# Optimization experiments

Measured on AMD Instinct MI355X. Metric: run time of the kernel, lower is better.

## Reference

```python
import math
import jax, jax.numpy as jnp
import numpy as np

EPS = 1.0
B, T, D, H = 8, 512, 768, 12
DH = D // H  # 64


def setup_inputs() -> dict:
    key = jax.random.key(0)
    ks = jax.random.split(key, 10)
    std = 0.02
    return {
        "x": jax.random.normal(ks[0], (B, T, D), dtype=jnp.float32),
        "r_position_embedding": jax.random.normal(ks[1], (T, D), dtype=jnp.float32),
        "r_content_bias": jax.random.normal(ks[2], (H, DH), dtype=jnp.float32),
        "r_position_bias": jax.random.normal(ks[3], (H, DH), dtype=jnp.float32),
        # Conv1D(linear) params, stored as (in, out) so y = x @ W + b
        "Wqkv": jax.random.normal(ks[4], (D, 3 * D), dtype=jnp.float32) * std,
        "bqkv": jnp.zeros((3 * D,), dtype=jnp.float32),
        "Wh": jax.random.normal(ks[5], (D, D), dtype=jnp.float32) * std,
        "bh": jnp.zeros((D,), dtype=jnp.float32),
        "Wp": jax.random.normal(ks[6], (D, D), dtype=jnp.float32) * std,
        "bp": jnp.zeros((D,), dtype=jnp.float32),
    }


def reference(x, r_position_embedding, r_content_bias, r_position_bias,
              Wqkv, bqkv, Wh, bh, Wp, bp):
    # QKV projection and head split
    qkv = x @ Wqkv + bqkv                                   # (B,T,3D)
    q, k, v = jnp.split(qkv, 3, axis=-1)
    split_heads = lambda t: t.reshape(B, T, H, DH).transpose(0, 2, 1, 3)  # (B,H,T,DH)
    q, k, v = split_heads(q), split_heads(k), split_heads(v)

    # content scores
    scores = jnp.einsum('bhtd,bhsd->bhts', q, k)            # (B,H,T,T)

    # relative position projection: linear is row-wise, so project once then gather.
    # rel_pos[c, r] = linear_position(pos_emb[max(0, c - r)])
    proj = (r_position_embedding @ Wp + bp).reshape(T, H, DH)  # (P=T, H, DH)
    idx = jnp.maximum(0, jnp.arange(T)[:, None] - jnp.arange(T)[None, :])  # (T,T) = max(0, c-r)

    # q . rel_pos term: compute vs all P distinct positions, then gather per (c, r)
    rel_q = jnp.einsum('bhtd,phd->bhtp', q, proj)           # (B,H,T,P)
    scores = scores + jnp.take_along_axis(rel_q, idx[None, None, :, :], axis=-1)

    # content-bias and position-bias terms (query-independent)
    bias_c = jnp.einsum('hd,phd->hp', r_content_bias, proj)[:, idx]   # (H,T,T)
    bias_p = jnp.einsum('hd,phd->hp', r_position_bias, proj)[:, idx]  # (H,T,T)
    scores = scores + bias_c[None] + bias_p[None]

    # masked softmax with EPS=1 quirks (faithful to original)
    scores = scores / (math.sqrt(DH) + EPS)
    mask = jnp.tril(jnp.ones((T, T), dtype=jnp.float32))    # causal
    masked_exps = jnp.exp(scores) * mask
    att = masked_exps / (masked_exps.sum(-1, keepdims=True) + 2.0 * EPS)

    ctx = jnp.einsum('bhts,bhsd->bhtd', att, v)             # (B,H,T,DH)
    # original: permute(0,2,3,1) then flatten -> (B,T,DH*H) interleaving (d, h)
    ctx = ctx.transpose(0, 2, 3, 1).reshape(B, T, D)
    out = ctx @ Wh + bh
    k_out = k.transpose(0, 1, 3, 2)                         # (B,H,DH,T) as module returns
    return out, k_out, v
```

## Files before the change

### kernel.cpp

```cpp
#include <hip/hip_runtime.h>
#include <hip/hip_bf16.h>


#define NT 512
#define ND 768
#define NH 12

typedef short short4_t __attribute__((ext_vector_type(4)));
typedef short short8_t __attribute__((ext_vector_type(8)));
typedef float float4_t __attribute__((ext_vector_type(4)));

__device__ __forceinline__ float b2f(unsigned short u) {
    union { unsigned int i; float f; } x; x.i = ((unsigned int)u) << 16; return x.f;
}
__device__ __forceinline__ unsigned short f2b(float f) {
    union { float f; unsigned int i; } x; x.f = f;
    unsigned int i = x.i;
    i += 0x7fffu + ((i >> 16) & 1u);
    return (unsigned short)(i >> 16);
}

__global__ __launch_bounds__(256) void cvt_b(const float* __restrict__ in,
                                             unsigned short* __restrict__ out, int n8)
{
    const int i = blockIdx.x * 256 + threadIdx.x;
    if (i >= n8) return;
    const float* s = in + (size_t)i * 8;
    float4_t f0 = *(const float4_t*)s;
    float4_t f1 = *(const float4_t*)(s + 4);
    union { short8_t v; unsigned short u[8]; } pk;
    pk.u[0] = f2b(f0[0]); pk.u[1] = f2b(f0[1]); pk.u[2] = f2b(f0[2]); pk.u[3] = f2b(f0[3]);
    pk.u[4] = f2b(f1[0]); pk.u[5] = f2b(f1[1]); pk.u[6] = f2b(f1[2]); pk.u[7] = f2b(f1[3]);
    *(short8_t*)&out[(size_t)i * 8] = pk.v;
}

__global__ __launch_bounds__(256) void transp_b(const float* __restrict__ in,
                                                unsigned short* __restrict__ out,
                                                int K, int N)
{
    __shared__ float t[32][33];
    const int k0 = blockIdx.y * 32;
    const int n0 = blockIdx.x * 32;
    const int r  = threadIdx.x >> 3;
    const int c  = (threadIdx.x & 7) * 4;
    float4_t v = *(const float4_t*)&in[(size_t)(k0 + r) * N + n0 + c];
    t[r][c + 0] = v[0]; t[r][c + 1] = v[1]; t[r][c + 2] = v[2]; t[r][c + 3] = v[3];
    __syncthreads();
    union { short4_t v; unsigned short u[4]; } pk;
    pk.u[0] = f2b(t[c + 0][r]);
    pk.u[1] = f2b(t[c + 1][r]);
    pk.u[2] = f2b(t[c + 2][r]);
    pk.u[3] = f2b(t[c + 3][r]);
    *(short4_t*)&out[(size_t)(n0 + r) * K + k0 + c] = pk.v;
}

template <int MODE>
__global__ __launch_bounds__(256) void gemm128(
    const unsigned short* __restrict__ A, const unsigned short* __restrict__ BT,
    const float* __restrict__ biasf,
    unsigned short* __restrict__ ob0, float* __restrict__ o1, float* __restrict__ o2,
    unsigned short* __restrict__ sh1, unsigned short* __restrict__ sh2,
    int K)
{
    __shared__ __attribute__((aligned(16))) unsigned short Al[2][128 * 32];
    __shared__ __attribute__((aligned(16))) unsigned short Bl[2][128 * 32];

    const int tid  = threadIdx.x;
    const int m0   = blockIdx.y * 128;
    const int n0   = blockIdx.x * 128;
    const int wave = tid >> 6;
    const int lane = tid & 63;
    const int lm   = lane & 15;
    const int quad = lane >> 4;
    const int wr   = (wave >> 1) * 64;
    const int wc   = (wave & 1) * 64;

    float4_t acc[4][4];
#pragma unroll
    for (int mt = 0; mt < 4; ++mt)
#pragma unroll
        for (int nt = 0; nt < 4; ++nt)
#pragma unroll
            for (int r = 0; r < 4; ++r) acc[mt][nt][r] = 0.f;

    const unsigned short* ap = A  + (size_t)(m0 + (tid >> 2)) * K + (tid & 3) * 8;
    const unsigned short* bp = BT + (size_t)(n0 + (tid >> 2)) * K + (tid & 3) * 8;
    const size_t rstep = (size_t)64 * K;

    auto stage = [&](int bi, int k0) {
        unsigned short* al0 = Al[bi] + wave * 512;
        unsigned short* bl0 = Bl[bi] + wave * 512;
        __builtin_amdgcn_global_load_lds(
            (const __attribute__((address_space(1))) void*)(ap + k0),
            (__attribute__((address_space(3))) void*)al0, 16, 0, 0);
        __builtin_amdgcn_global_load_lds(
            (const __attribute__((address_space(1))) void*)(ap + rstep + k0),
            (__attribute__((address_space(3))) void*)(al0 + 2048), 16, 0, 0);
        __builtin_amdgcn_global_load_lds(
            (const __attribute__((address_space(1))) void*)(bp + k0),
            (__attribute__((address_space(3))) void*)bl0, 16, 0, 0);
        __builtin_amdgcn_global_load_lds(
            (const __attribute__((address_space(1))) void*)(bp + rstep + k0),
            (__attribute__((address_space(3))) void*)(bl0 + 2048), 16, 0, 0);
    };

    stage(0, 0);
    asm volatile("s_waitcnt vmcnt(0)" ::: "memory");
    __builtin_amdgcn_s_barrier();

    int cur = 0;
    for (int k0 = 0; k0 < K; k0 += 32) {
        if (k0 + 32 < K) stage(cur ^ 1, k0 + 32);

        short8_t af[4], bf[4];
#pragma unroll
        for (int mt = 0; mt < 4; ++mt)
            af[mt] = *(const short8_t*)&Al[cur][(wr + mt * 16 + lm) * 32 + quad * 8];
#pragma unroll
        for (int nt = 0; nt < 4; ++nt)
            bf[nt] = *(const short8_t*)&Bl[cur][(wc + nt * 16 + lm) * 32 + quad * 8];
#pragma unroll
        for (int mt = 0; mt < 4; ++mt)
#pragma unroll
            for (int nt = 0; nt < 4; ++nt)
                acc[mt][nt] = __builtin_amdgcn_mfma_f32_16x16x32_bf16(af[mt], bf[nt], acc[mt][nt], 0, 0, 0);

        asm volatile("s_waitcnt vmcnt(0)" ::: "memory");
        __builtin_amdgcn_s_barrier();
        cur ^= 1;
    }

#pragma unroll
    for (int nt = 0; nt < 4; ++nt) {
        const int gcol = n0 + wc + nt * 16 + lm;
        const float bv = biasf[gcol];
#pragma unroll
        for (int mt = 0; mt < 4; ++mt) {
#pragma unroll
            for (int r = 0; r < 4; ++r) {
                const int grow = m0 + wr + mt * 16 + quad * 4 + r;
                const float val = acc[mt][nt][r] + bv;
                if (MODE == 0) {
                    int b = grow >> 9, t = grow & 511;
                    int sec = gcol / 768;
                    int cc = gcol - sec * 768;
                    int h = cc >> 6, d = cc & 63;
                    if (sec == 0) {
                        ob0[((size_t)((b * NH + h) * NT + t)) * 64 + d] = f2b(val);
                    } else if (sec == 1) {
                        o1[((size_t)((b * NH + h) * 64 + d)) * NT + t] = val;
                        sh1[((size_t)((b * NH + h) * NT + t)) * 64 + d] = f2b(val);
                    } else {
                        o2[((size_t)((b * NH + h) * NT + t)) * 64 + d] = val;
                        sh2[((size_t)((b * NH + h) * 64 + d)) * NT + t] = f2b(val);
                    }
                } else {
                    o1[(size_t)grow * ND + gcol] = val;
                }
            }
        }
    }
}

template <int MODE>
__global__ __launch_bounds__(256) void gemm_mfma(
    const float* __restrict__ Af, const unsigned short* __restrict__ Ab,
    const float* __restrict__ Bw, const float* __restrict__ biasf,
    unsigned short* __restrict__ ob0, float* __restrict__ o1, float* __restrict__ o2,
    int N, int K, int ldb)
{
    __shared__ unsigned short Al[64][40];
    __shared__ unsigned short Bl[64][40];

    const int tid  = threadIdx.x;
    const int m0   = blockIdx.y * 64;
    const int n0   = blockIdx.x * 64;
    const int wave = tid >> 6;
    const int lane = tid & 63;
    const int lm   = lane & 15;
    const int quad = lane >> 4;
    const int koff = quad * 8;

    float4_t acc[4];
#pragma unroll
    for (int j = 0; j < 4; ++j)
#pragma unroll
        for (int r = 0; r < 4; ++r) acc[j][r] = 0.0f;

    const int arow = tid >> 2;
    const int acg  = (tid & 3) * 8;
    const int bk   = tid & 31;
    const int bg   = tid >> 5;

    for (int k0 = 0; k0 < K; k0 += 32) {
        {
            const float* src = &Af[(size_t)(m0 + arow) * K + k0 + acg];
            float4_t f0 = *(const float4_t*)src;
            float4_t f1 = *(const float4_t*)(src + 4);
            union { short8_t v; unsigned short u[8]; } pk;
            pk.u[0] = f2b(f0[0]); pk.u[1] = f2b(f0[1]); pk.u[2] = f2b(f0[2]); pk.u[3] = f2b(f0[3]);
            pk.u[4] = f2b(f1[0]); pk.u[5] = f2b(f1[1]); pk.u[6] = f2b(f1[2]); pk.u[7] = f2b(f1[3]);
            *(short8_t*)&Al[arow][acg] = pk.v;
        }
        {
            const float* src = &Bw[(size_t)(k0 + bk) * ldb + n0 + bg * 8];
            float4_t f0 = *(const float4_t*)src;
            float4_t f1 = *(const float4_t*)(src + 4);
            Bl[bg * 8 + 0][bk] = f2b(f0[0]); Bl[bg * 8 + 1][bk] = f2b(f0[1]);
            Bl[bg * 8 + 2][bk] = f2b(f0[2]); Bl[bg * 8 + 3][bk] = f2b(f0[3]);
            Bl[bg * 8 + 4][bk] = f2b(f1[0]); Bl[bg * 8 + 5][bk] = f2b(f1[1]);
            Bl[bg * 8 + 6][bk] = f2b(f1[2]); Bl[bg * 8 + 7][bk] = f2b(f1[3]);
        }
        __syncthreads();

        short8_t af = *(const short8_t*)&Al[wave * 16 + lm][koff];
#pragma unroll
        for (int j = 0; j < 4; ++j) {
            short8_t bf = *(const short8_t*)&Bl[j * 16 + lm][koff];
            acc[j] = __builtin_amdgcn_mfma_f32_16x16x32_bf16(af, bf, acc[j], 0, 0, 0);
        }
        __syncthreads();
    }

#pragma unroll
    for (int j = 0; j < 4; ++j) {
        const int gcol = n0 + j * 16 + lm;
        const float bv = biasf[gcol];
#pragma unroll
        for (int r = 0; r < 4; ++r) {
            const int grow = m0 + wave * 16 + quad * 4 + r;
            const float val = acc[j][r] + bv;
            if (MODE == 1) {
                int h = gcol >> 6, d = gcol & 63;
                ob0[((size_t)(h * NT + grow)) * 64 + d] = f2b(val);
            }
        }
    }
}

__global__ __launch_bounds__(256) void biascp_kernel(
    const float* __restrict__ rcb, const float* __restrict__ rpb,
    const unsigned short* __restrict__ projb, float* __restrict__ biascp)
{
    __shared__ float cb[64];
    const int h = blockIdx.x;
    const int tid = threadIdx.x;
    if (tid < 64) cb[tid] = rcb[h * 64 + tid] + rpb[h * 64 + tid];
    __syncthreads();
    for (int p = tid; p < NT; p += 256) {
        const unsigned short* pr = &projb[((size_t)(h * NT + p)) * 64];
        float s = 0.f;
#pragma unroll 8
        for (int d = 0; d < 64; ++d) s += b2f(pr[d]) * cb[d];
        biascp[h * NT + p] = s;
    }
}

__global__ __launch_bounds__(128) void attn_mfma(
    const unsigned short* __restrict__ q_ws, const unsigned short* __restrict__ k_ws,
    const unsigned short* __restrict__ v_ws, const unsigned short* __restrict__ projb,
    const float* __restrict__ biascp, unsigned short* __restrict__ ctxT)
{
    __shared__ unsigned short Kt[64][72];
    __shared__ unsigned short Vt[64][72];
    __shared__ unsigned short pP[96][72];
    __shared__ float          Rl[2][16][84];
    __shared__ unsigned short esl[2][16][72];

    const int tid   = threadIdx.x;
    const int y     = blockIdx.y;
    const int h     = y % NH;
    const int b     = y / NH;
    const int pairi = blockIdx.x;
    const int wave  = tid >> 6;
    const int lane  = tid & 63;
    const int lm    = lane & 15;
    const int quad  = lane >> 4;
    const int koff  = quad * 8;

    const int sr = tid >> 1;
    const int sc = (tid & 1) * 32;

    for (int c = 0; c < 2; ++c) {
        const int ti  = c ? pairi : (15 - pairi);
        const int tb0 = ti * 32;
        const int tw0 = tb0 + wave * 16;
        const int nst = (tb0 >> 6) + 1;

        short8_t aq[2];
        aq[0] = *(const short8_t*)&q_ws[((size_t)(y * NT + tw0 + lm)) * 64 + koff];
        aq[1] = *(const short8_t*)&q_ws[((size_t)(y * NT + tw0 + lm)) * 64 + koff + 32];

        float4_t ctxacc[4];
#pragma unroll
        for (int j = 0; j < 4; ++j)
#pragma unroll
            for (int r = 0; r < 4; ++r) ctxacc[j][r] = 0.f;
        float esum[4] = {0.f, 0.f, 0.f, 0.f};

        for (int st = 0; st < nst; ++st) {
            const int s0      = st * 64;
            const int plo_blk = max(0, tb0 - s0 - 63);
            const int cnt_blk = tb0 + 31 - s0 - plo_blk + 1;
            if (c | st) __syncthreads();
            {
                const unsigned short* ks = &k_ws[((size_t)(y * NT + s0 + sr)) * 64 + sc];
                *(short8_t*)&Kt[sr][sc]      = *(const short8_t*)ks;
                *(short8_t*)&Kt[sr][sc + 8]  = *(const short8_t*)(ks + 8);
                *(short8_t*)&Kt[sr][sc + 16] = *(const short8_t*)(ks + 16);
                *(short8_t*)&Kt[sr][sc + 24] = *(const short8_t*)(ks + 24);
                const unsigned short* vs = &v_ws[((size_t)(y * 64 + sr)) * NT + s0 + sc];
                *(short8_t*)&Vt[sr][sc]      = *(const short8_t*)vs;
                *(short8_t*)&Vt[sr][sc + 8]  = *(const short8_t*)(vs + 8);
                *(short8_t*)&Vt[sr][sc + 16] = *(const short8_t*)(vs + 16);
                *(short8_t*)&Vt[sr][sc + 24] = *(const short8_t*)(vs + 24);
                for (int p = tid; p < cnt_blk; p += 128) {
                    const unsigned short* ps = &projb[((size_t)(h * NT + plo_blk + p)) * 64];
                    *(short8_t*)&pP[p][0]  = *(const short8_t*)ps;
                    *(short8_t*)&pP[p][8]  = *(const short8_t*)(ps + 8);
                    *(short8_t*)&pP[p][16] = *(const short8_t*)(ps + 16);
                    *(short8_t*)&pP[p][24] = *(const short8_t*)(ps + 24);
                    *(short8_t*)&pP[p][32] = *(const short8_t*)(ps + 32);
                    *(short8_t*)&pP[p][40] = *(const short8_t*)(ps + 40);
                    *(short8_t*)&pP[p][48] = *(const short8_t*)(ps + 48);
                    *(short8_t*)&pP[p][56] = *(const short8_t*)(ps + 56);
                }
            }
            __syncthreads();

            if (s0 <= tw0 + 15) {
                const int plo_w = max(0, tw0 - s0 - 63);
                const int pbase = plo_w - plo_blk;
                const int cntw  = tw0 + 15 - s0 - plo_w + 1;
                const int jmax  = min(3, (tw0 + 15 - s0) >> 4);
                const int jpmax = (cntw - 1) >> 4;

                float4_t accQK[4];
#pragma unroll
                for (int j = 0; j < 4; ++j)
#pragma unroll
                    for (int r = 0; r < 4; ++r) accQK[j][r] = 0.f;
                for (int j = 0; j <= jmax; ++j) {
                    short8_t bk0 = *(const short8_t*)&Kt[j * 16 + lm][koff];
                    short8_t bk1 = *(const short8_t*)&Kt[j * 16 + lm][koff + 32];
                    accQK[j] = __builtin_amdgcn_mfma_f32_16x16x32_bf16(aq[0], bk0, accQK[j], 0, 0, 0);
                    accQK[j] = __builtin_amdgcn_mfma_f32_16x16x32_bf16(aq[1], bk1, accQK[j], 0, 0, 0);
                }
                for (int j = 0; j <= jpmax; ++j) {
                    short8_t bp0 = *(const short8_t*)&pP[pbase + j * 16 + lm][koff];
                    short8_t bp1 = *(const short8_t*)&pP[pbase + j * 16 + lm][koff + 32];
                    float4_t accR;
#pragma unroll
                    for (int r = 0; r < 4; ++r) accR[r] = 0.f;
                    accR = __builtin_amdgcn_mfma_f32_16x16x32_bf16(aq[0], bp0, accR, 0, 0, 0);
                    accR = __builtin_amdgcn_mfma_f32_16x16x32_bf16(aq[1], bp1, accR, 0, 0, 0);
                    const int p = j * 16 + lm;
                    const float bv = biascp[h * NT + min(plo_w + p, NT - 1)];
#pragma unroll
                    for (int r = 0; r < 4; ++r) Rl[wave][quad * 4 + r][p] = accR[r] + bv;
                }
                asm volatile("" ::: "memory");

#pragma unroll
                for (int j = 0; j < 4; ++j) {
                    const int s_g = s0 + j * 16 + lm;
#pragma unroll
                    for (int r = 0; r < 4; ++r) {
                        const int t_g = tw0 + quad * 4 + r;
                        float e = 0.f;
                        if (s_g <= t_g) {
                            const int p = t_g - s_g - plo_w;
                            e = __expf(fminf((accQK[j][r] + Rl[wave][quad * 4 + r][p]) * (1.f / 9.f), 60.f));
                        }
                        esl[wave][quad * 4 + r][j * 16 + lm] = f2b(e);
                        esum[r] += e;
                    }
                }
                asm volatile("" ::: "memory");

                short8_t ae0 = *(const short8_t*)&esl[wave][lm][koff];
                short8_t ae1 = *(const short8_t*)&esl[wave][lm][koff + 32];
#pragma unroll
                for (int j = 0; j < 4; ++j) {
                    short8_t bv0 = *(const short8_t*)&Vt[j * 16 + lm][koff];
                    short8_t bv1 = *(const short8_t*)&Vt[j * 16 + lm][koff + 32];
                    ctxacc[j] = __builtin_amdgcn_mfma_f32_16x16x32_bf16(ae0, bv0, ctxacc[j], 0, 0, 0);
                    ctxacc[j] = __builtin_amdgcn_mfma_f32_16x16x32_bf16(ae1, bv1, ctxacc[j], 0, 0, 0);
                }
            }
        }

        float rcpv[4];
#pragma unroll
        for (int r = 0; r < 4; ++r) {
            float v = esum[r];
            v += __shfl_xor(v, 1); v += __shfl_xor(v, 2);
            v += __shfl_xor(v, 4); v += __shfl_xor(v, 8);
            rcpv[r] = 1.f / (v + 2.f);
        }
#pragma unroll
        for (int j = 0; j < 4; ++j) {
            const int d = j * 16 + lm;
#pragma unroll
            for (int r = 0; r < 4; ++r) {
                const int t = tw0 + quad * 4 + r;
                ctxT[((size_t)(b * NT + t)) * ND + d * NH + h] = f2b(ctxacc[j][r] * rcpv[r]);
            }
        }
    }
}

extern "C" void kernel_launch(void* const* d_in, const int* in_sizes, int n_in,
                              void* d_out, int out_size, void* d_ws, size_t ws_size,
                              hipStream_t stream)
{
    const float* x    = (const float*)d_in[0];
    const float* rpe  = (const float*)d_in[1];
    const float* rcb  = (const float*)d_in[2];
    const float* rpb  = (const float*)d_in[3];
    const float* Wqkv = (const float*)d_in[4];
    const float* bqkv = (const float*)d_in[5];
    const float* Wh   = (const float*)d_in[6];
    const float* bh   = (const float*)d_in[7];
    const float* Wp   = (const float*)d_in[8];
    const float* bp   = (const float*)d_in[9];

    float* out  = (float*)d_out;
    float* kout = out + 3145728;
    float* vout = out + 6291456;

    unsigned short* q_ws  = (unsigned short*)d_ws;
    unsigned short* k_ws  = q_ws + 3145728;
    unsigned short* v_ws  = k_ws + 3145728;
    unsigned short* ctxT  = v_ws + 3145728;
    unsigned short* xb    = ctxT;
    unsigned short* projb = ctxT + 3145728;
    float* biascp = (float*)(projb + 393216);
    unsigned short* WqkvT = (unsigned short*)(biascp + 6144);
    unsigned short* WhT   = WqkvT + 1769472;

    cvt_b<<<dim3(1536), 256, 0, stream>>>(x, xb, 393216);
    transp_b<<<dim3(2304 / 32, 768 / 32), 256, 0, stream>>>(Wqkv, WqkvT, 768, 2304);
    transp_b<<<dim3(768 / 32, 768 / 32), 256, 0, stream>>>(Wh, WhT, 768, 768);

    gemm128<0><<<dim3(2304 / 128, 4096 / 128), 256, 0, stream>>>(
        xb, WqkvT, bqkv, q_ws, kout, vout, k_ws, v_ws, 768);
    gemm_mfma<1><<<dim3(768 / 64, 512 / 64), 256, 0, stream>>>(
        rpe, nullptr, Wp, bp, projb, nullptr, nullptr, 768, 768, 768);
    biascp_kernel<<<dim3(12), 256, 0, stream>>>(rcb, rpb, projb, biascp);
    attn_mfma<<<dim3(8, 96), 128, 0, stream>>>(
        q_ws, k_ws, v_ws, projb, biascp, ctxT);
    gemm128<2><<<dim3(768 / 128, 4096 / 128), 256, 0, stream>>>(
        ctxT, WhT, bh, nullptr, out, nullptr, nullptr, nullptr, 768);
}
```

Measured before the change: 239.3 us.

## Merge prep kernels, triple-buffer GEMM loads, fuse bias dot into projection GEMM

Merges the x conversion and the two weight transposes into a single prep launch, and folds the content/position bias reduction into the epilogue of the position-projection GEMM using a wave shuffle reduction, removing two launches. The 128x128 GEMM moves from double to triple buffering in LDS with a partial vmcnt wait, so loads run two stages ahead and each iteration needs one barrier instead of two. This uses more LDS per block, which may lower occupancy, and biascp is now computed from unrounded fp32 values rather than the bf16 projection.

```diff
diff --git a/kernel.cpp b/kernel.cpp
--- a/kernel.cpp
+++ b/kernel.cpp
@@ -20,29 +20,38 @@
     return (unsigned short)(i >> 16);
 }
 
-__global__ __launch_bounds__(256) void cvt_b(const float* __restrict__ in,
-                                             unsigned short* __restrict__ out, int n8)
-{
-    const int i = blockIdx.x * 256 + threadIdx.x;
-    if (i >= n8) return;
-    const float* s = in + (size_t)i * 8;
-    float4_t f0 = *(const float4_t*)s;
-    float4_t f1 = *(const float4_t*)(s + 4);
-    union { short8_t v; unsigned short u[8]; } pk;
-    pk.u[0] = f2b(f0[0]); pk.u[1] = f2b(f0[1]); pk.u[2] = f2b(f0[2]); pk.u[3] = f2b(f0[3]);
-    pk.u[4] = f2b(f1[0]); pk.u[5] = f2b(f1[1]); pk.u[6] = f2b(f1[2]); pk.u[7] = f2b(f1[3]);
-    *(short8_t*)&out[(size_t)i * 8] = pk.v;
-}
-
-__global__ __launch_bounds__(256) void transp_b(const float* __restrict__ in,
-                                                unsigned short* __restrict__ out,
-                                                int K, int N)
+__global__ __launch_bounds__(256) void prep(
+    const float* __restrict__ x, unsigned short* __restrict__ xb,
+    const float* __restrict__ Wqkv, unsigned short* __restrict__ WqkvT,
+    const float* __restrict__ Wh, unsigned short* __restrict__ WhT)
 {
     __shared__ float t[32][33];
-    const int k0 = blockIdx.y * 32;
-    const int n0 = blockIdx.x * 32;
-    const int r  = threadIdx.x >> 3;
-    const int c  = (threadIdx.x & 7) * 4;
+    const int bid = blockIdx.x;
+    const int tid = threadIdx.x;
+
+    if (bid < 1536) {
+        const int i = bid * 256 + tid;
+        const float* s = x + (size_t)i * 8;
+        float4_t f0 = *(const float4_t*)s;
+        float4_t f1 = *(const float4_t*)(s + 4);
+        union { short8_t v; unsigned short u[8]; } pk;
+        pk.u[0] = f2b(f0[0]); pk.u[1] = f2b(f0[1]); pk.u[2] = f2b(f0[2]); pk.u[3] = f2b(f0[3]);
+        pk.u[4] = f2b(f1[0]); pk.u[5] = f2b(f1[1]); pk.u[6] = f2b(f1[2]); pk.u[7] = f2b(f1[3]);
+        *(short8_t*)&xb[(size_t)i * 8] = pk.v;
+        return;
+    }
+    const float* in; unsigned short* out; int K, N, k0, n0;
+    if (bid < 3264) {
+        const int tt = bid - 1536;
+        in = Wqkv; out = WqkvT; K = 768; N = 2304;
+        n0 = (tt % 72) * 32; k0 = (tt / 72) * 32;
+    } else {
+        const int tt = bid - 3264;
+        in = Wh; out = WhT; K = 768; N = 768;
+        n0 = (tt % 24) * 32; k0 = (tt / 24) * 32;
+    }
+    const int r = tid >> 3;
+    const int c = (tid & 7) * 4;
     float4_t v = *(const float4_t*)&in[(size_t)(k0 + r) * N + n0 + c];
     t[r][c + 0] = v[0]; t[r][c + 1] = v[1]; t[r][c + 2] = v[2]; t[r][c + 3] = v[3];
     __syncthreads();
@@ -62,8 +71,8 @@
     unsigned short* __restrict__ sh1, unsigned short* __restrict__ sh2,
     int K)
 {
-    __shared__ __attribute__((aligned(16))) unsigned short Al[2][128 * 32];
-    __shared__ __attribute__((aligned(16))) unsigned short Bl[2][128 * 32];
+    __shared__ __attribute__((aligned(16))) unsigned short Al[3][128 * 32];
+    __shared__ __attribute__((aligned(16))) unsigned short Bl[3][128 * 32];
 
     const int tid  = threadIdx.x;
     const int m0   = blockIdx.y * 128;
@@ -88,8 +97,8 @@
     const size_t rstep = (size_t)64 * K;
 
     auto stage = [&](int bi, int k0) {
-        unsigned short* al0 = Al[bi] + wave * 512;
-        unsigned short* bl0 = Bl[bi] + wave * 512;
+        unsigned short* al0 = &Al[bi][0] + wave * 512;
+        unsigned short* bl0 = &Bl[bi][0] + wave * 512;
         __builtin_amdgcn_global_load_lds(
             (const __attribute__((address_space(1))) void*)(ap + k0),
             (__attribute__((address_space(3))) void*)al0, 16, 0, 0);
@@ -105,12 +114,16 @@
     };
 
     stage(0, 0);
-    asm volatile("s_waitcnt vmcnt(0)" ::: "memory");
-    __builtin_amdgcn_s_barrier();
+    stage(1, 32);
 
     int cur = 0;
     for (int k0 = 0; k0 < K; k0 += 32) {
-        if (k0 + 32 < K) stage(cur ^ 1, k0 + 32);
+        if (k0 + 32 < K) asm volatile("s_waitcnt vmcnt(4)" ::: "memory");
+        else             asm volatile("s_waitcnt vmcnt(0)" ::: "memory");
+        __builtin_amdgcn_s_barrier();
+        __builtin_amdgcn_sched_barrier(0);
+
+        if (k0 + 64 < K) stage((cur + 2) % 3, k0 + 64);
 
         short8_t af[4], bf[4];
 #pragma unroll
@@ -125,9 +138,7 @@
             for (int nt = 0; nt < 4; ++nt)
                 acc[mt][nt] = __builtin_amdgcn_mfma_f32_16x16x32_bf16(af[mt], bf[nt], acc[mt][nt], 0, 0, 0);
 
-        asm volatile("s_waitcnt vmcnt(0)" ::: "memory");
-        __builtin_amdgcn_s_barrier();
-        cur ^= 1;
+        cur = (cur + 1) % 3;
     }
 
 #pragma unroll
@@ -162,12 +173,11 @@
     }
 }
 
-template <int MODE>
-__global__ __launch_bounds__(256) void gemm_mfma(
-    const float* __restrict__ Af, const unsigned short* __restrict__ Ab,
-    const float* __restrict__ Bw, const float* __restrict__ biasf,
-    unsigned short* __restrict__ ob0, float* __restrict__ o1, float* __restrict__ o2,
-    int N, int K, int ldb)
+__global__ __launch_bounds__(256) void gemm_proj(
+    const float* __restrict__ Af, const float* __restrict__ Bw,
+    const float* __restrict__ biasf,
+    const float* __restrict__ rcb, const float* __restrict__ rpb,
+    unsigned short* __restrict__ projb, float* __restrict__ biascp)
 {
     __shared__ unsigned short Al[64][40];
     __shared__ unsigned short Bl[64][40];
@@ -180,6 +190,7 @@
     const int lm   = lane & 15;
     const int quad = lane >> 4;
     const int koff = quad * 8;
+    const int K = 768, ldb = 768;
 
     float4_t acc[4];
 #pragma unroll
@@ -222,37 +233,32 @@
         __syncthreads();
     }
 
+    const int h = n0 >> 6;
+    float cb4[4], part[4] = {0.f, 0.f, 0.f, 0.f};
+#pragma unroll
+    for (int j = 0; j < 4; ++j) {
+        const int d = j * 16 + lm;
+        cb4[j] = rcb[h * 64 + d] + rpb[h * 64 + d];
+    }
 #pragma unroll
     for (int j = 0; j < 4; ++j) {
         const int gcol = n0 + j * 16 + lm;
+        const int d = gcol & 63;
         const float bv = biasf[gcol];
 #pragma unroll
         for (int r = 0; r < 4; ++r) {
             const int grow = m0 + wave * 16 + quad * 4 + r;
             const float val = acc[j][r] + bv;
-            if (MODE == 1) {
-                int h = gcol >> 6, d = gcol & 63;
-                ob0[((size_t)(h * NT + grow)) * 64 + d] = f2b(val);
-            }
-        }
-    }
-}
-
-__global__ __launch_bounds__(256) void biascp_kernel(
-    const float* __restrict__ rcb, const float* __restrict__ rpb,
-    const unsigned short* __restrict__ projb, float* __restrict__ biascp)
-{
-    __shared__ float cb[64];
-    const int h = blockIdx.x;
-    const int tid = threadIdx.x;
-    if (tid < 64) cb[tid] = rcb[h * 64 + tid] + rpb[h * 64 + tid];
-    __syncthreads();
-    for (int p = tid; p < NT; p += 256) {
-        const unsigned short* pr = &projb[((size_t)(h * NT + p)) * 64];
-        float s = 0.f;
-#pragma unroll 8
-        for (int d = 0; d < 64; ++d) s += b2f(pr[d]) * cb[d];
-        biascp[h * NT + p] = s;
+            projb[((size_t)(h * NT + grow)) * 64 + d] = f2b(val);
+            part[r] += val * cb4[j];
+        }
+    }
+#pragma unroll
+    for (int r = 0; r < 4; ++r) {
+        float v = part[r];
+        v += __shfl_xor(v, 1); v += __shfl_xor(v, 2);
+        v += __shfl_xor(v, 4); v += __shfl_xor(v, 8);
+        if (lm == 0) biascp[h * NT + m0 + wave * 16 + quad * 4 + r] = v;
     }
 }
 
@@ -439,15 +445,12 @@
     unsigned short* WqkvT = (unsigned short*)(biascp + 6144);
     unsigned short* WhT   = WqkvT + 1769472;
 
-    cvt_b<<<dim3(1536), 256, 0, stream>>>(x, xb, 393216);
-    transp_b<<<dim3(2304 / 32, 768 / 32), 256, 0, stream>>>(Wqkv, WqkvT, 768, 2304);
-    transp_b<<<dim3(768 / 32, 768 / 32), 256, 0, stream>>>(Wh, WhT, 768, 768);
+    prep<<<dim3(3840), 256, 0, stream>>>(x, xb, Wqkv, WqkvT, Wh, WhT);
 
     gemm128<0><<<dim3(2304 / 128, 4096 / 128), 256, 0, stream>>>(
         xb, WqkvT, bqkv, q_ws, kout, vout, k_ws, v_ws, 768);
-    gemm_mfma<1><<<dim3(768 / 64, 512 / 64), 256, 0, stream>>>(
-        rpe, nullptr, Wp, bp, projb, nullptr, nullptr, 768, 768, 768);
-    biascp_kernel<<<dim3(12), 256, 0, stream>>>(rcb, rpb, projb, biascp);
+    gemm_proj<<<dim3(768 / 64, 512 / 64), 256, 0, stream>>>(
+        rpe, Wp, bp, rcb, rpb, projb, biascp);
     attn_mfma<<<dim3(8, 96), 128, 0, stream>>>(
         q_ws, k_ws, v_ws, projb, biascp, ctxT);
     gemm128<2><<<dim3(768 / 128, 4096 / 128), 256, 0, stream>>>(
```

New measurement: 239.0 us. About the same (-0.1%).
